# Optimization experiments

Measured on AMD Instinct MI355X. Metric: run time of the kernel, lower is better.

## Reference

```python
import jax, jax.numpy as jnp
import numpy as np

N = 100000
E = 800000
D_IN = 128
D_OUT = 128
EPS = 1e-5


def setup_inputs() -> dict:
    key = jax.random.key(0)
    k = jax.random.split(key, 7)
    x = jax.random.normal(k[0], (N, D_IN), dtype=jnp.float32)
    edge_index = jax.random.randint(k[1], (2, E), 0, N, dtype=jnp.int64)
    # kaiming_uniform(a=sqrt(5)) on [out,in] -> bound = 1/sqrt(in_dim)
    bound = 1.0 / np.sqrt(D_IN)
    W_self = jax.random.uniform(k[2], (D_OUT, D_IN), minval=-bound, maxval=bound, dtype=jnp.float32)
    W_neigh = jax.random.uniform(k[3], (D_OUT, D_IN), minval=-bound, maxval=bound, dtype=jnp.float32)
    bias = jnp.zeros((D_OUT,), dtype=jnp.float32)
    gamma = jnp.ones((D_OUT,), dtype=jnp.float32)
    beta = jnp.zeros((D_OUT,), dtype=jnp.float32)
    return {"x": x, "edge_index": edge_index, "W_self": W_self,
            "W_neigh": W_neigh, "bias": bias, "gamma": gamma, "beta": beta}


def reference(x, edge_index, W_self, W_neigh, bias, gamma, beta):
    src, dst = edge_index[0], edge_index[1]
    # mean neighbor aggregation: segment-sum of gathered features / clamped degree
    agg = jax.ops.segment_sum(x[src], dst, num_segments=N)          # [N, D_IN]
    deg = jax.ops.segment_sum(jnp.ones_like(dst, dtype=x.dtype), dst, num_segments=N)
    neigh_mean = agg / jnp.maximum(deg, 1.0)[:, None]
    # dual linear + bias + ReLU
    out = jnp.einsum('nd,od->no', x, W_self) + jnp.einsum('nd,od->no', neigh_mean, W_neigh) + bias
    h = jax.nn.relu(out)
    # LayerNorm over last dim
    mu = jnp.mean(h, axis=-1, keepdims=True)
    var = jnp.var(h, axis=-1, keepdims=True)
    return (h - mu) * jax.lax.rsqrt(var + EPS) * gamma + beta
```

## Files before the change

kernel.cpp:

```cpp
#include <hip/hip_runtime.h>
#include <hip/hip_bf16.h>

#define N_NODES 100000
#define E_EDGES 800000
#define LN_EPS 1e-5f
#define WPAD 264

#define P_BLOCKS 256
#define EPB 3125
#define SLICE 64
#define NBK 1563
#define NBK_PAD 1792
#define OFFS_STRIDE 1564
#define QCAP 768
#define CONV_PER_BLOCK 12500

typedef __attribute__((ext_vector_type(4))) float f32x4;
typedef __attribute__((ext_vector_type(8))) short short8;

__device__ __forceinline__ unsigned short f2bf(float f) {
    __hip_bfloat16 h = __float2bfloat16(f);
    return *reinterpret_cast<unsigned short*>(&h);
}
__device__ __forceinline__ float bflo(unsigned int u) { return __uint_as_float(u << 16); }
__device__ __forceinline__ float bfhi(unsigned int u) { return __uint_as_float(u & 0xffff0000u); }

__global__ __launch_bounds__(256) void fill_part1(
    const float* __restrict__ x, const int* __restrict__ ei,
    unsigned short* __restrict__ xb, unsigned int* __restrict__ gstore,
    unsigned short* __restrict__ offs)
{
    const int t = threadIdx.x, b = blockIdx.x;
    if (b >= P_BLOCKS) {
        const float4* x4 = reinterpret_cast<const float4*>(x);
        ushort4* xb4 = reinterpret_cast<ushort4*>(xb);
        const int j0 = (b - P_BLOCKS) * CONV_PER_BLOCK;
        for (int j = t; j < CONV_PER_BLOCK; j += 256) {
            float4 v = x4[j0 + j];
            ushort4 o;
            o.x = f2bf(v.x); o.y = f2bf(v.y); o.z = f2bf(v.z); o.w = f2bf(v.w);
            xb4[j0 + j] = o;
        }
        return;
    }
    __shared__ unsigned long long eds[EPB];
    __shared__ unsigned int sorted_l[EPB];
    __shared__ int hist[NBK_PAD];
    __shared__ int starts[NBK_PAD + 1];
    __shared__ int partial[256];
    for (int i = t; i < NBK_PAD; i += 256) hist[i] = 0;
    __syncthreads();
    const int e0 = b * EPB;
    for (int i = t; i < EPB; i += 256) {
        unsigned src = (unsigned)ei[e0 + i];
        unsigned dst = (unsigned)ei[E_EDGES + e0 + i];
        unsigned bk = dst >> 6;
        eds[i] = ((unsigned long long)bk << 32) | (src << 6) | (dst & 63u);
        atomicAdd(&hist[bk], 1);
    }
    __syncthreads();
    int h[7], s = 0;
#pragma unroll
    for (int k = 0; k < 7; ++k) { h[k] = hist[t * 7 + k]; s += h[k]; }
    partial[t] = s;
    __syncthreads();
    for (int off = 1; off < 256; off <<= 1) {
        int v = (t >= off) ? partial[t - off] : 0;
        __syncthreads();
        partial[t] += v;
        __syncthreads();
    }
    int run = partial[t] - s;
#pragma unroll
    for (int k = 0; k < 7; ++k) { starts[t * 7 + k] = run; run += h[k]; }
    if (t == 255) starts[NBK_PAD] = run;
    __syncthreads();
    for (int i = t; i < NBK_PAD; i += 256) hist[i] = 0;
    __syncthreads();
    for (int i = t; i < EPB; i += 256) {
        unsigned long long u = eds[i];
        unsigned bk = (unsigned)(u >> 32);
        int p = starts[bk] + atomicAdd(&hist[bk], 1);
        sorted_l[p] = (unsigned int)u;
    }
    __syncthreads();
    for (int i = t; i < EPB; i += 256)
        gstore[b * EPB + i] = sorted_l[i];
    for (int i = t; i < OFFS_STRIDE; i += 256)
        offs[b * OFFS_STRIDE + i] = (unsigned short)starts[i];
}

__global__ __launch_bounds__(256) void agg2(
    const unsigned int* __restrict__ gstore, const unsigned short* __restrict__ offs,
    const unsigned short* __restrict__ xb, unsigned short* __restrict__ nb)
{
    __shared__ unsigned int sortedq[QCAP];
    __shared__ int cnt_l[SLICE];
    __shared__ int run_l[SLICE];
    __shared__ int qs_l[SLICE + 1];
    const int t = threadIdx.x, b = blockIdx.x;
    if (t < SLICE) { cnt_l[t] = 0; run_l[t] = 0; }
    __syncthreads();
    const int s0 = offs[t * OFFS_STRIDE + b];
    const int s1 = offs[t * OFFS_STRIDE + b + 1];
    const unsigned int* myrun = gstore + t * EPB;
    for (int j = s0; j < s1; ++j)
        atomicAdd(&cnt_l[myrun[j] & 63u], 1);
    __syncthreads();
    if (t < SLICE) {
        int inc = cnt_l[t];
        for (int off = 1; off < 64; off <<= 1) {
            int u = __shfl_up(inc, off);
            if (t >= off) inc += u;
        }
        qs_l[t + 1] = inc;
        if (t == 0) qs_l[0] = 0;
    }
    __syncthreads();
    for (int j = s0; j < s1; ++j) {
        unsigned rec = myrun[j];
        int p = qs_l[rec & 63u] + atomicAdd(&run_l[rec & 63u], 1);
        if (p < QCAP) sortedq[p] = rec;
    }
    __syncthreads();
    const int wave = t >> 6, lane = t & 63;
    const int subi = lane >> 4, chunk = lane & 15;
    const uint4* x4 = reinterpret_cast<const uint4*>(xb);
    for (int ln = wave * 16; ln < wave * 16 + 16; ++ln) {
        const int qb = qs_l[ln], cc = qs_l[ln + 1] - qb;
        float acc[8];
#pragma unroll
        for (int k = 0; k < 8; ++k) acc[k] = 0.f;
        for (int i = 0; i < cc; i += 4) {
            int idx = i + subi;
            if (idx < cc) {
                unsigned rec = sortedq[qb + idx];
                uint4 v = x4[(rec >> 6) * 16 + chunk];
                acc[0] += bflo(v.x); acc[1] += bfhi(v.x);
                acc[2] += bflo(v.y); acc[3] += bfhi(v.y);
                acc[4] += bflo(v.z); acc[5] += bfhi(v.z);
                acc[6] += bflo(v.w); acc[7] += bfhi(v.w);
            }
        }
#pragma unroll
        for (int k = 0; k < 8; ++k) {
            acc[k] += __shfl_xor(acc[k], 16);
            acc[k] += __shfl_xor(acc[k], 32);
        }
        const int node = b * SLICE + ln;
        if (subi == 0 && node < N_NODES) {
            float inv = 1.0f / (float)(cc > 1 ? cc : 1);
            uint4 o;
            o.x = ((unsigned)f2bf(acc[1] * inv) << 16) | f2bf(acc[0] * inv);
            o.y = ((unsigned)f2bf(acc[3] * inv) << 16) | f2bf(acc[2] * inv);
            o.z = ((unsigned)f2bf(acc[5] * inv) << 16) | f2bf(acc[4] * inv);
            o.w = ((unsigned)f2bf(acc[7] * inv) << 16) | f2bf(acc[6] * inv);
            reinterpret_cast<uint4*>(nb)[node * 16 + chunk] = o;
        }
    }
}

__global__ __launch_bounds__(256, 2) void fused_mfma(
    const unsigned short* __restrict__ xb, const unsigned short* __restrict__ nb,
    const float* __restrict__ Wself, const float* __restrict__ Wneigh,
    const float* __restrict__ bias, const float* __restrict__ gamma,
    const float* __restrict__ beta, float* __restrict__ out)
{
    __shared__ unsigned short WT[128][WPAD];
    const int t = threadIdx.x;
    const float4* Ws4 = reinterpret_cast<const float4*>(Wself);
    const float4* Wn4 = reinterpret_cast<const float4*>(Wneigh);
    for (int idx = t; idx < 4096; idx += 256) {
        int n = idx >> 5, k4 = (idx & 31) << 2;
        float4 a = Ws4[idx];
        float4 b = Wn4[idx];
        ushort4 ua, ub;
        ua.x = f2bf(a.x); ua.y = f2bf(a.y); ua.z = f2bf(a.z); ua.w = f2bf(a.w);
        ub.x = f2bf(b.x); ub.y = f2bf(b.y); ub.z = f2bf(b.z); ub.w = f2bf(b.w);
        *reinterpret_cast<ushort4*>(&WT[n][k4]) = ua;
        *reinterpret_cast<ushort4*>(&WT[n][128 + k4]) = ub;
    }
    __syncthreads();

    const int lane = t & 63, wave = t >> 6;
    const int l16 = lane & 15, quad = lane >> 4;
    float bia[8], gam[8], bet[8];
#pragma unroll
    for (int n = 0; n < 8; ++n) {
        int col = n * 16 + l16;
        bia[n] = bias[col]; gam[n] = gamma[col]; bet[n] = beta[col];
    }

    const int ntiles = (N_NODES + 255) / 256;
    for (int tile = blockIdx.x; tile < ntiles; tile += gridDim.x) {
        const int rowbase = tile * 256 + wave * 64;
        f32x4 acc[4][8];
#pragma unroll
        for (int m = 0; m < 4; ++m)
#pragma unroll
            for (int n = 0; n < 8; ++n) acc[m][n] = (f32x4)0.f;
        int rows[4];
#pragma unroll
        for (int m = 0; m < 4; ++m) {
            int r = rowbase + m * 16 + l16;
            rows[m] = r < N_NODES ? r : N_NODES - 1;
        }
#pragma unroll
        for (int kstep = 0; kstep < 8; ++kstep) {
            const unsigned short* Asrc = (kstep < 4) ? xb : nb;
            const int koff = (kstep & 3) * 32 + quad * 8;
            short8 a[4];
#pragma unroll
            for (int m = 0; m < 4; ++m)
                a[m] = *reinterpret_cast<const short8*>(Asrc + rows[m] * 128 + koff);
#pragma unroll
            for (int n = 0; n < 8; ++n) {
                short8 b = *reinterpret_cast<const short8*>(&WT[n * 16 + l16][kstep * 32 + quad * 8]);
#pragma unroll
                for (int m = 0; m < 4; ++m)
                    acc[m][n] = __builtin_amdgcn_mfma_f32_16x16x32_bf16(a[m], b, acc[m][n], 0, 0, 0);
            }
        }
#pragma unroll
        for (int m = 0; m < 4; ++m) {
#pragma unroll
            for (int r = 0; r < 4; ++r) {
                float h[8], s = 0.f, q = 0.f;
#pragma unroll
                for (int n = 0; n < 8; ++n) {
                    float v = acc[m][n][r] + bia[n];
                    v = fmaxf(v, 0.f);
                    h[n] = v; s += v; q += v * v;
                }
#pragma unroll
                for (int msk = 1; msk <= 8; msk <<= 1) {
                    s += __shfl_xor(s, msk);
                    q += __shfl_xor(q, msk);
                }
                const float mu = s * (1.f / 128.f);
                const float var = q * (1.f / 128.f) - mu * mu;
                const float rs = rsqrtf(var + LN_EPS);
                const int R = rowbase + m * 16 + quad * 4 + r;
                if (R < N_NODES) {
#pragma unroll
                    for (int n = 0; n < 8; ++n)
                        out[R * 128 + n * 16 + l16] = (h[n] - mu) * rs * gam[n] + bet[n];
                }
            }
        }
    }
}

extern "C" void kernel_launch(void* const* d_in, const int* in_sizes, int n_in,
                              void* d_out, int out_size, void* d_ws, size_t ws_size,
                              hipStream_t stream) {
    const float* x      = (const float*)d_in[0];
    const int*   ei     = (const int*)d_in[1];
    const float* Wself  = (const float*)d_in[2];
    const float* Wneigh = (const float*)d_in[3];
    const float* bias   = (const float*)d_in[4];
    const float* gamma  = (const float*)d_in[5];
    const float* beta   = (const float*)d_in[6];
    float* out = (float*)d_out;

    char* ws = (char*)d_ws;
    unsigned short* xb = (unsigned short*)ws;
    unsigned short* nb = (unsigned short*)(ws + 25600000);
    unsigned int* gstore = (unsigned int*)(ws + 51200000);
    unsigned short* offs = (unsigned short*)(ws + 54400000);

    fill_part1<<<512, 256, 0, stream>>>(x, ei, xb, gstore, offs);
    agg2<<<NBK, 256, 0, stream>>>(gstore, offs, xb, nb);
    const int ntiles = (N_NODES + 255) / 256;
    fused_mfma<<<ntiles, 256, 0, stream>>>(xb, nb, Wself, Wneigh, bias, gamma, beta, out);
}
```

Measured before the change: 204.8 us.

## Double partition blocks, split aggregation feature halves across blocks, simplify local sort

The edge partition now runs on 512 blocks of about 1563 edges each instead of 256 blocks of 3125. The local counting sort is rewritten to read dst twice instead of staging packed 64-bit records, and it uses a wave-shuffle scan in place of the barrier-heavy shared-memory scan. The aggregation kernel launches twice as many blocks, and each one handles half of the 128 feature columns for its 64-node slice. This raises parallelism and shortens per-thread gather chains. The cost is that each aggregation block repeats the per-slice bucket scan over 512 runs, doubling that bookkeeping overall.

```diff
diff --git a/kernel.cpp b/kernel.cpp
--- a/kernel.cpp
+++ b/kernel.cpp
@@ -6,8 +6,8 @@
 #define LN_EPS 1e-5f
 #define WPAD 264
 
-#define P_BLOCKS 256
-#define EPB 3125
+#define P_BLOCKS 512
+#define EPB 1563
 #define SLICE 64
 #define NBK 1563
 #define NBK_PAD 1792
@@ -43,51 +43,49 @@
         }
         return;
     }
-    __shared__ unsigned long long eds[EPB];
     __shared__ unsigned int sorted_l[EPB];
     __shared__ int hist[NBK_PAD];
-    __shared__ int starts[NBK_PAD + 1];
-    __shared__ int partial[256];
+    __shared__ int wsum[4];
+    const int lane = t & 63, wid = t >> 6;
+    const int e0 = b * EPB;
+    const int ne = (e0 + EPB <= E_EDGES) ? EPB : (E_EDGES - e0);
     for (int i = t; i < NBK_PAD; i += 256) hist[i] = 0;
     __syncthreads();
-    const int e0 = b * EPB;
-    for (int i = t; i < EPB; i += 256) {
+    for (int i = t; i < ne; i += 256)
+        atomicAdd(&hist[((unsigned)ei[E_EDGES + e0 + i]) >> 6], 1);
+    __syncthreads();
+    int h[7], s = 0;
+#pragma unroll
+    for (int k = 0; k < 7; ++k) { h[k] = hist[t * 7 + k]; s += h[k]; }
+    int inc = s;
+#pragma unroll
+    for (int off = 1; off < 64; off <<= 1) {
+        int u = __shfl_up(inc, off);
+        if (lane >= off) inc += u;
+    }
+    if (lane == 63) wsum[wid] = inc;
+    __syncthreads();
+    int wbase = 0;
+#pragma unroll
+    for (int w = 0; w < 4; ++w) if (w < wid) wbase += wsum[w];
+    int run = wbase + inc - s;
+#pragma unroll
+    for (int k = 0; k < 7; ++k) {
+        int idx = t * 7 + k;
+        if (idx < OFFS_STRIDE) offs[b * OFFS_STRIDE + idx] = (unsigned short)run;
+        hist[idx] = run;
+        run += h[k];
+    }
+    __syncthreads();
+    for (int i = t; i < ne; i += 256) {
         unsigned src = (unsigned)ei[e0 + i];
         unsigned dst = (unsigned)ei[E_EDGES + e0 + i];
-        unsigned bk = dst >> 6;
-        eds[i] = ((unsigned long long)bk << 32) | (src << 6) | (dst & 63u);
-        atomicAdd(&hist[bk], 1);
-    }
-    __syncthreads();
-    int h[7], s = 0;
-#pragma unroll
-    for (int k = 0; k < 7; ++k) { h[k] = hist[t * 7 + k]; s += h[k]; }
-    partial[t] = s;
-    __syncthreads();
-    for (int off = 1; off < 256; off <<= 1) {
-        int v = (t >= off) ? partial[t - off] : 0;
-        __syncthreads();
-        partial[t] += v;
-        __syncthreads();
-    }
-    int run = partial[t] - s;
-#pragma unroll
-    for (int k = 0; k < 7; ++k) { starts[t * 7 + k] = run; run += h[k]; }
-    if (t == 255) starts[NBK_PAD] = run;
-    __syncthreads();
-    for (int i = t; i < NBK_PAD; i += 256) hist[i] = 0;
-    __syncthreads();
-    for (int i = t; i < EPB; i += 256) {
-        unsigned long long u = eds[i];
-        unsigned bk = (unsigned)(u >> 32);
-        int p = starts[bk] + atomicAdd(&hist[bk], 1);
-        sorted_l[p] = (unsigned int)u;
-    }
-    __syncthreads();
-    for (int i = t; i < EPB; i += 256)
+        int p = atomicAdd(&hist[dst >> 6], 1);
+        sorted_l[p] = (src << 6) | (dst & 63u);
+    }
+    __syncthreads();
+    for (int i = t; i < ne; i += 256)
         gstore[b * EPB + i] = sorted_l[i];
-    for (int i = t; i < OFFS_STRIDE; i += 256)
-        offs[b * OFFS_STRIDE + i] = (unsigned short)starts[i];
 }
 
 __global__ __launch_bounds__(256) void agg2(
@@ -98,14 +96,23 @@
     __shared__ int cnt_l[SLICE];
     __shared__ int run_l[SLICE];
     __shared__ int qs_l[SLICE + 1];
-    const int t = threadIdx.x, b = blockIdx.x;
+    const int t = threadIdx.x;
+    const int b = blockIdx.x >> 1, half = blockIdx.x & 1;
     if (t < SLICE) { cnt_l[t] = 0; run_l[t] = 0; }
     __syncthreads();
-    const int s0 = offs[t * OFFS_STRIDE + b];
-    const int s1 = offs[t * OFFS_STRIDE + b + 1];
-    const unsigned int* myrun = gstore + t * EPB;
-    for (int j = s0; j < s1; ++j)
-        atomicAdd(&cnt_l[myrun[j] & 63u], 1);
+    int s0[2], s1[2];
+#pragma unroll
+    for (int u = 0; u < 2; ++u) {
+        int rr = t + u * 256;
+        s0[u] = offs[rr * OFFS_STRIDE + b];
+        s1[u] = offs[rr * OFFS_STRIDE + b + 1];
+    }
+#pragma unroll
+    for (int u = 0; u < 2; ++u) {
+        const unsigned int* myrun = gstore + (t + u * 256) * EPB;
+        for (int j = s0[u]; j < s1[u]; ++j)
+            atomicAdd(&cnt_l[myrun[j] & 63u], 1);
+    }
     __syncthreads();
     if (t < SLICE) {
         int inc = cnt_l[t];
@@ -117,25 +124,30 @@
         if (t == 0) qs_l[0] = 0;
     }
     __syncthreads();
-    for (int j = s0; j < s1; ++j) {
-        unsigned rec = myrun[j];
-        int p = qs_l[rec & 63u] + atomicAdd(&run_l[rec & 63u], 1);
-        if (p < QCAP) sortedq[p] = rec;
+#pragma unroll
+    for (int u = 0; u < 2; ++u) {
+        const unsigned int* myrun = gstore + (t + u * 256) * EPB;
+        for (int j = s0[u]; j < s1[u]; ++j) {
+            unsigned rec = myrun[j];
+            int p = qs_l[rec & 63u] + atomicAdd(&run_l[rec & 63u], 1);
+            if (p < QCAP) sortedq[p] = rec;
+        }
     }
     __syncthreads();
     const int wave = t >> 6, lane = t & 63;
-    const int subi = lane >> 4, chunk = lane & 15;
+    const int subi = lane >> 3, chunk = lane & 7;
+    const int cbase = half * 8;
     const uint4* x4 = reinterpret_cast<const uint4*>(xb);
     for (int ln = wave * 16; ln < wave * 16 + 16; ++ln) {
         const int qb = qs_l[ln], cc = qs_l[ln + 1] - qb;
         float acc[8];
 #pragma unroll
         for (int k = 0; k < 8; ++k) acc[k] = 0.f;
-        for (int i = 0; i < cc; i += 4) {
+        for (int i = 0; i < cc; i += 8) {
             int idx = i + subi;
-            if (idx < cc) {
+            if (idx < cc && qb + idx < QCAP) {
                 unsigned rec = sortedq[qb + idx];
-                uint4 v = x4[(rec >> 6) * 16 + chunk];
+                uint4 v = x4[(rec >> 6) * 16 + cbase + chunk];
                 acc[0] += bflo(v.x); acc[1] += bfhi(v.x);
                 acc[2] += bflo(v.y); acc[3] += bfhi(v.y);
                 acc[4] += bflo(v.z); acc[5] += bfhi(v.z);
@@ -144,6 +156,7 @@
         }
 #pragma unroll
         for (int k = 0; k < 8; ++k) {
+            acc[k] += __shfl_xor(acc[k], 8);
             acc[k] += __shfl_xor(acc[k], 16);
             acc[k] += __shfl_xor(acc[k], 32);
         }
@@ -155,7 +168,7 @@
             o.y = ((unsigned)f2bf(acc[3] * inv) << 16) | f2bf(acc[2] * inv);
             o.z = ((unsigned)f2bf(acc[5] * inv) << 16) | f2bf(acc[4] * inv);
             o.w = ((unsigned)f2bf(acc[7] * inv) << 16) | f2bf(acc[6] * inv);
-            reinterpret_cast<uint4*>(nb)[node * 16 + chunk] = o;
+            reinterpret_cast<uint4*>(nb)[node * 16 + cbase + chunk] = o;
         }
     }
 }
@@ -267,10 +280,10 @@
     unsigned short* xb = (unsigned short*)ws;
     unsigned short* nb = (unsigned short*)(ws + 25600000);
     unsigned int* gstore = (unsigned int*)(ws + 51200000);
-    unsigned short* offs = (unsigned short*)(ws + 54400000);
-
-    fill_part1<<<512, 256, 0, stream>>>(x, ei, xb, gstore, offs);
-    agg2<<<NBK, 256, 0, stream>>>(gstore, offs, xb, nb);
+    unsigned short* offs = (unsigned short*)(ws + 54401024);
+
+    fill_part1<<<P_BLOCKS + 256, 256, 0, stream>>>(x, ei, xb, gstore, offs);
+    agg2<<<2 * NBK, 256, 0, stream>>>(gstore, offs, xb, nb);
     const int ntiles = (N_NODES + 255) / 256;
     fused_mfma<<<ntiles, 256, 0, stream>>>(xb, nb, Wself, Wneigh, bias, gamma, beta, out);
 }
```

Result: slower. 239.2 us (+16.8%).
